# Optimization experiments

Hardware: AMD Instinct MI355X
Metric: run time of the kernel (lower is better)

Reference implementation:

```python
import jax, jax.numpy as jnp
import numpy as np

TAU = 2.0  # gumbel-softmax temperature (hard=False)


def setup_inputs() -> dict:
    key = jax.random.key(0)
    k = jax.random.split(key, 6)
    b = 128
    names = jax.random.normal(k[0], (b, 256, 30, 32), jnp.float32)
    patterns = jax.random.normal(k[1], (b, 4, 128, 128), jnp.float32)
    attributes = jax.random.normal(k[2], (b, 8, 15, 16), jnp.float32)
    palettes = jax.random.normal(k[3], (b, 8, 12), jnp.float32)
    u1 = jax.random.uniform(k[4], (b, 960, 256), jnp.float32, 1e-6, 1.0 - 1e-6)
    u2 = jax.random.uniform(k[5], (b, 240, 8), jnp.float32, 1e-6, 1.0 - 1e-6)
    gumbel_names = -jnp.log(-jnp.log(u1))
    gumbel_attrs = -jnp.log(-jnp.log(u2))
    return {"names": names, "patterns": patterns, "attributes": attributes,
            "palettes": palettes, "gumbel_names": gumbel_names, "gumbel_attrs": gumbel_attrs}


def reference(names, patterns, attributes, palettes, gumbel_names, gumbel_attrs):
    b = names.shape[0]
    # tile-name logits: (b,256,30,32) -> (b, 960 tiles, 256 names)
    n = names.reshape(b, 256, 30 * 32).transpose(0, 2, 1)
    names_idxs = jax.nn.softmax((n + gumbel_names) / TAU, axis=-1)
    # pattern table: (b,4,128,128) -> 256 tiles of 8x8 pixels x 4 gray levels
    p = patterns.reshape(b, 4, 16, 8, 16, 8).transpose(0, 2, 4, 3, 5, 1)
    p = jax.nn.softmax(p, axis=-1).reshape(b, 256, 8 * 8 * 4)
    # attribute logits: (b,8,15,16) -> (b, 240 blocks, 8 palettes)
    a = attributes.reshape(b, 8, 15 * 16).transpose(0, 2, 1)
    attributes_idxs = jax.nn.softmax((a + gumbel_attrs) / TAU, axis=-1)
    pal = palettes.reshape(b, 8, 4 * 3)
    # soft tile lookup: (b,960,256) @ (b,256,256) -> (b,960,256)
    monochrome = jnp.einsum('btn,bnp->btp', names_idxs, p)
    monochrome = monochrome.reshape(b, 30 * 32, 8 * 8, 4, 1)
    # soft palette lookup: (b,240,8) @ (b,8,12) -> (b,240,12)
    colorization = jnp.einsum('bte,bec->btc', attributes_idxs, pal)
    colorization = colorization.reshape(b, 15, 16, 4, 3)
    # 2x2 attribute-block broadcast to the 30x32 nametable
    colorization = jnp.repeat(jnp.repeat(colorization, 2, axis=1), 2, axis=2)
    colorization = colorization.reshape(b, 30 * 32, 1, 4, 3)
    colorized = (monochrome * colorization).sum(axis=3)  # (b,960,64,3)
    image = colorized.reshape(b, 30, 32, 8, 8, 3).transpose(0, 5, 1, 3, 2, 4)
    image = image.reshape(b, 3, 30 * 8, 32 * 8)
    image = jax.nn.sigmoid(image)
    return image, names_idxs, p, attributes_idxs, pal
```

## Files before the change

### kernel.cpp

```cpp
#include <hip/hip_runtime.h>
#include <hip/hip_bf16.h>
#include <math.h>

#define O_IMG   0
#define O_NAMES 23592960ULL
#define O_P     55050240ULL
#define O_ATTR  63438848ULL
#define O_PAL   63684608ULL

typedef __attribute__((ext_vector_type(8))) short short8v;
typedef __attribute__((ext_vector_type(4))) float f32x4;

static __device__ inline unsigned short f2bf(float x) {
    __hip_bfloat16 h = __float2bfloat16(x);
    return *reinterpret_cast<unsigned short*>(&h);
}

template<bool WRITE_PT>
__global__ __launch_bounds__(256) void k_pattern2(const float* __restrict__ patterns,
                                                  float* __restrict__ out_p,
                                                  unsigned short* __restrict__ Pt) {
    int bp = blockIdx.x;
    int b  = bp >> 3;
    int pi = bp & 7;

    __shared__ float sP[4 * 16 * 136];
    __shared__ unsigned short sR[32 * 264];

    int tid = threadIdx.x;

    #pragma unroll
    for (int p = 0; p < 8; p++) {
        int li   = p * 256 + tid;
        int col4 = li & 31;
        int ti   = (li >> 5) & 15;
        int g    = li >> 9;
        float4 v = *(const float4*)(patterns + (size_t)b * 65536 + g * 16384 +
                                    (ti * 8 + pi) * 128 + col4 * 4);
        *(float4*)&sP[(g * 16 + ti) * 136 + col4 * 4] = v;
    }
    __syncthreads();

    int pj = tid & 7;
    int nb = tid >> 3;
    #pragma unroll
    for (int i = 0; i < 8; i++) {
        int n  = nb * 8 + i;
        int ti = n >> 4, tj = n & 15;
        int base = ti * 136 + tj * 8 + pj;
        float v0 = sP[              base];
        float v1 = sP[16 * 136   + base];
        float v2 = sP[32 * 136   + base];
        float v3 = sP[48 * 136   + base];
        float m  = fmaxf(fmaxf(v0, v1), fmaxf(v2, v3));
        float e0 = __expf(v0 - m), e1 = __expf(v1 - m), e2 = __expf(v2 - m), e3 = __expf(v3 - m);
        float inv = 1.0f / (e0 + e1 + e2 + e3);
        float p0 = e0 * inv, p1 = e1 * inv, p2 = e2 * inv, p3 = e3 * inv;
        float4 r; r.x = p0; r.y = p1; r.z = p2; r.w = p3;
        *(float4*)(out_p + (size_t)(b * 256 + n) * 256 + pi * 32 + pj * 4) = r;
        if (WRITE_PT) {
            sR[(pj * 4 + 0) * 264 + n] = f2bf(p0);
            sR[(pj * 4 + 1) * 264 + n] = f2bf(p1);
            sR[(pj * 4 + 2) * 264 + n] = f2bf(p2);
            sR[(pj * 4 + 3) * 264 + n] = f2bf(p3);
        }
    }
    if (WRITE_PT) {
        __syncthreads();
        int n4  = tid & 63;
        int fl0 = tid >> 6;
        #pragma unroll
        for (int k = 0; k < 8; k++) {
            int fl = fl0 * 8 + k;
            short4 rv = *(short4*)&sR[fl * 264 + n4 * 4];
            *(short4*)(Pt + (size_t)b * 65536 + (size_t)(pi * 32 + fl) * 256 + n4 * 4) = rv;
        }
    }
}

__global__ __launch_bounds__(256) void k_names(const float* __restrict__ names,
                                               const float* __restrict__ gumbel,
                                               float* __restrict__ out) {
    int chunk = blockIdx.x % 60;
    int b     = blockIdx.x / 60;
    int t0 = chunk * 16;
    __shared__ float sN[256 * 17];

    int q = threadIdx.x;
    const float* nb = names + (size_t)b * 245760 + t0;
    {
        int j  = q & 3;
        int n0 = q >> 2;
        #pragma unroll
        for (int pass = 0; pass < 4; pass++) {
            int n = n0 + 64 * pass;
            float4 v = *(const float4*)(nb + (size_t)n * 960 + 4 * j);
            float* dst = sN + n * 17 + 4 * j;
            dst[0] = v.x; dst[1] = v.y; dst[2] = v.z; dst[3] = v.w;
        }
    }
    __syncthreads();

    int lane = q & 63;
    int w    = q >> 6;
    const float* gb = gumbel + ((size_t)b * 960 + t0) * 256;
    float*       ob = out    + ((size_t)b * 960 + t0) * 256;

    #pragma unroll
    for (int tt = 0; tt < 4; tt++) {
        int t = w * 4 + tt;
        float v[4];
        #pragma unroll
        for (int k = 0; k < 4; k++) {
            int n = lane + 64 * k;
            v[k] = (sN[n * 17 + t] + gb[(size_t)t * 256 + n]) * 0.5f;
        }
        float m = fmaxf(fmaxf(v[0], v[1]), fmaxf(v[2], v[3]));
        #pragma unroll
        for (int off = 1; off < 64; off <<= 1) m = fmaxf(m, __shfl_xor(m, off));
        float s = 0.f;
        #pragma unroll
        for (int k = 0; k < 4; k++) { v[k] = expf(v[k] - m); s += v[k]; }
        #pragma unroll
        for (int off = 1; off < 64; off <<= 1) s += __shfl_xor(s, off);
        float inv = 1.0f / s;
        #pragma unroll
        for (int k = 0; k < 4; k++) ob[(size_t)t * 256 + lane + 64 * k] = v[k] * inv;
    }
}

__global__ __launch_bounds__(256) void k_attr(const float* __restrict__ attributes,
                                              const float* __restrict__ gumbel,
                                              const float* __restrict__ palettes,
                                              float* __restrict__ out_attr,
                                              float* __restrict__ out_pal) {
    int idx = blockIdx.x * 256 + threadIdx.x;
    if (idx < 12288) out_pal[idx] = palettes[idx];
    if (idx >= 128 * 240) return;
    int tb = idx % 240;
    int b  = idx / 240;
    float v[8];
    float m = -1e30f;
    #pragma unroll
    for (int e = 0; e < 8; e++) {
        v[e] = (attributes[((size_t)b * 8 + e) * 240 + tb] +
                gumbel[((size_t)b * 240 + tb) * 8 + e]) * 0.5f;
        m = fmaxf(m, v[e]);
    }
    float s = 0.f;
    #pragma unroll
    for (int e = 0; e < 8; e++) { v[e] = __expf(v[e] - m); s += v[e]; }
    float inv = 1.0f / s;
    float* o = out_attr + (size_t)idx * 8;
    #pragma unroll
    for (int e = 0; e < 8; e++) o[e] = v[e] * inv;
}

__global__ __launch_bounds__(256, 4) void k_fused(const float* __restrict__ names,
                                                  const float* __restrict__ gumbel,
                                                  const unsigned short* __restrict__ Pt,
                                                  const float* __restrict__ attr,
                                                  const float* __restrict__ pal,
                                                  float* __restrict__ out_names,
                                                  float* __restrict__ img) {
    int j  = blockIdx.x;
    int x  = j & 7;
    int s  = j >> 3;
    int q  = s / 30;
    int rr = s % 30;
    int b  = x + 8 * q;
    int t0 = rr * 32;

    __shared__ __align__(16) char smem[16896];
    __shared__ float sN[256 * 17];
    __shared__ float sCol[192];

    int tid  = threadIdx.x;
    int lane = tid & 63;
    int w    = tid >> 6;
    int lo   = lane & 15;
    int hi   = lane >> 4;

    if (tid < 192) {
        int tbl = tid / 12;
        int gc  = tid % 12;
        int tb  = (rr >> 1) * 16 + tbl;
        const float* at = attr + ((size_t)b * 240 + tb) * 8;
        const float* pl = pal + (size_t)b * 96 + gc;
        float sum = 0.f;
        #pragma unroll
        for (int e = 0; e < 8; e++) sum += at[e] * pl[e * 12];
        sCol[tbl * 12 + gc] = sum;
    }

    const float* nb  = names + (size_t)b * 245760 + t0;
    const float* gb  = gumbel + ((size_t)b * 960 + t0) * 256;
    float*       onb = out_names + ((size_t)b * 960 + t0) * 256;

    for (int c = 0; c < 2; c++) {
        if (c) __syncthreads();
        {
            int jj = tid & 3;
            int n0 = tid >> 2;
            #pragma unroll
            for (int p = 0; p < 4; p++) {
                int n = n0 + 64 * p;
                float4 v = *(const float4*)(nb + (size_t)n * 960 + c * 16 + 4 * jj);
                float* dst = sN + n * 17 + 4 * jj;
                dst[0] = v.x; dst[1] = v.y; dst[2] = v.z; dst[3] = v.w;
            }
        }
        __syncthreads();
        #pragma unroll
        for (int tt = 0; tt < 4; tt++) {
            int trow = w * 4 + tt;
            int tl   = c * 16 + trow;
            float v[4];
            #pragma unroll
            for (int k = 0; k < 4; k++) {
                int n = lane + 64 * k;
                v[k] = (sN[n * 17 + trow] + gb[(size_t)tl * 256 + n]) * 0.5f;
            }
            float m = fmaxf(fmaxf(v[0], v[1]), fmaxf(v[2], v[3]));
            #pragma unroll
            for (int off = 1; off < 64; off <<= 1) m = fmaxf(m, __shfl_xor(m, off));
            float sm = 0.f;
            #pragma unroll
            for (int k = 0; k < 4; k++) { v[k] = __expf(v[k] - m); sm += v[k]; }
            #pragma unroll
            for (int off = 1; off < 64; off <<= 1) sm += __shfl_xor(sm, off);
            float inv = 1.0f / sm;
            #pragma unroll
            for (int k = 0; k < 4; k++) {
                int n = lane + 64 * k;
                float p = v[k] * inv;
                onb[(size_t)tl * 256 + n] = p;
                *(unsigned short*)(smem + ((tl * 512 + n * 2) ^ ((tl & 7) << 4))) = f2bf(p);
            }
        }
    }
    __syncthreads();

    f32x4 acc[2][4];
    #pragma unroll
    for (int mi = 0; mi < 2; mi++)
        #pragma unroll
        for (int ni = 0; ni < 4; ni++) acc[mi][ni] = (f32x4){0.f, 0.f, 0.f, 0.f};

    const unsigned short* Ptb = Pt + (size_t)b * 65536 + hi * 8;

    short8v bcur[4], bnxt[4];
    #pragma unroll
    for (int ni = 0; ni < 4; ni++) {
        int f = w * 64 + ni * 16 + lo;
        bcur[ni] = *(const short8v*)(Ptb + (size_t)f * 256);
    }

    #pragma unroll
    for (int k0 = 0; k0 < 256; k0 += 32) {
        if (k0 < 224) {
            #pragma unroll
            for (int ni = 0; ni < 4; ni++) {
                int f = w * 64 + ni * 16 + lo;
                bnxt[ni] = *(const short8v*)(Ptb + (size_t)f * 256 + k0 + 32);
            }
        }
        int ka = (k0 + hi * 8) * 2;
        short8v a0 = *(short8v*)(smem + (((lo      ) * 512 + ka) ^ ((lo & 7) << 4)));
        short8v a1 = *(short8v*)(smem + (((lo + 16) * 512 + ka) ^ ((lo & 7) << 4)));
        #pragma unroll
        for (int ni = 0; ni < 4; ni++) {
            acc[0][ni] = __builtin_amdgcn_mfma_f32_16x16x32_bf16(a0, bcur[ni], acc[0][ni], 0, 0, 0);
            acc[1][ni] = __builtin_amdgcn_mfma_f32_16x16x32_bf16(a1, bcur[ni], acc[1][ni], 0, 0, 0);
        }
        if (k0 < 224) {
            #pragma unroll
            for (int ni = 0; ni < 4; ni++) bcur[ni] = bnxt[ni];
        }
    }

    float* sMono = (float*)smem;
    int tf = tid & 63;
    int tm = tid >> 6;
    int pi = tf >> 3, pj = tf & 7;

    #pragma unroll
    for (int mi = 0; mi < 2; mi++) {
        __syncthreads();
        #pragma unroll
        for (int ni = 0; ni < 4; ni++) {
            int colf = w * 64 + ni * 16 + lo;
            #pragma unroll
            for (int rg = 0; rg < 4; rg++)
                sMono[(hi * 4 + rg) * 260 + colf] = acc[mi][ni][rg];
        }
        __syncthreads();
        int cbase = mi * 16;
        #pragma unroll
        for (int i = 0; i < 4; i++) {
            int ccl  = tm * 4 + i;
            int ccol = cbase + ccl;
            int tbl  = ccol >> 1;
            float4 mv = *(float4*)&sMono[ccl * 260 + tf * 4];
            #pragma unroll
            for (int c = 0; c < 3; c++) {
                float sv = mv.x * sCol[tbl * 12 + c]
                         + mv.y * sCol[tbl * 12 + 3 + c]
                         + mv.z * sCol[tbl * 12 + 6 + c]
                         + mv.w * sCol[tbl * 12 + 9 + c];
                float y = 1.0f / (1.0f + __expf(-sv));
                img[(((size_t)b * 3 + c) * 240 + rr * 8 + pi) * 256 + ccol * 8 + pj] = y;
            }
        }
    }
}

__global__ __launch_bounds__(256) void k_image_fp32(const float* __restrict__ A,
                                                    const float* __restrict__ P,
                                                    const float* __restrict__ attr,
                                                    const float* __restrict__ pal,
                                                    float* __restrict__ img) {
    int blk = blockIdx.x;
    int r = blk % 30;
    int b = blk / 30;
    int t0 = r * 32;

    __shared__ float sA[32][33];
    __shared__ float sB[32][256];
    __shared__ float sColF[16][12];

    int tid = threadIdx.x;
    if (tid < 192) {
        int tbl = tid / 12;
        int gc  = tid % 12;
        int tb  = (r >> 1) * 16 + tbl;
        const float* at = attr + ((size_t)b * 240 + tb) * 8;
        const float* pl = pal + (size_t)b * 96 + gc;
        float s = 0.f;
        #pragma unroll
        for (int e = 0; e < 8; e++) s += at[e] * pl[e * 12];
        sColF[tbl][gc] = s;
    }

    float acc[8][4];
    #pragma unroll
    for (int i = 0; i < 8; i++)
        #pragma unroll
        for (int j = 0; j < 4; j++) acc[i][j] = 0.f;

    int tf = tid & 63;
    int tm = tid >> 6;

    const float* Ab = A + ((size_t)b * 960 + t0) * 256;
    const float* Pb = P + (size_t)b * 65536;

    for (int k0 = 0; k0 < 256; k0 += 32) {
        __syncthreads();
        #pragma unroll
        for (int i = 0; i < 4; i++) {
            int li = tid + i * 256;
            int tl = li >> 5, kk = li & 31;
            sA[tl][kk] = Ab[(size_t)tl * 256 + k0 + kk];
        }
        #pragma unroll
        for (int i = 0; i < 8; i++) {
            int li = tid + i * 256;
            int kk = li >> 6, ff = (li & 63) * 4;
            *(float4*)&sB[kk][ff] = *(const float4*)&Pb[(size_t)(k0 + kk) * 256 + ff];
        }
        __syncthreads();
        #pragma unroll
        for (int kk = 0; kk < 32; kk++) {
            float4 bv = *(float4*)&sB[kk][tf * 4];
            #pragma unroll
            for (int i = 0; i < 8; i++) {
                float av = sA[tm * 8 + i][kk];
                acc[i][0] += av * bv.x;
                acc[i][1] += av * bv.y;
                acc[i][2] += av * bv.z;
                acc[i][3] += av * bv.w;
            }
        }
    }

    int pi = tf >> 3, pj = tf & 7;
    #pragma unroll
    for (int i = 0; i < 8; i++) {
        int cc  = tm * 8 + i;
        int tbl = cc >> 1;
        #pragma unroll
        for (int c = 0; c < 3; c++) {
            float s = acc[i][0] * sColF[tbl][c]
                    + acc[i][1] * sColF[tbl][3 + c]
                    + acc[i][2] * sColF[tbl][6 + c]
                    + acc[i][3] * sColF[tbl][9 + c];
            float y = 1.0f / (1.0f + expf(-s));
            img[(((size_t)b * 3 + c) * 240 + r * 8 + pi) * 256 + cc * 8 + pj] = y;
        }
    }
}

extern "C" void kernel_launch(void* const* d_in, const int* in_sizes, int n_in,
                              void* d_out, int out_size, void* d_ws, size_t ws_size,
                              hipStream_t stream) {
    const float* names       = (const float*)d_in[0];
    const float* patterns    = (const float*)d_in[1];
    const float* attributes  = (const float*)d_in[2];
    const float* palettes    = (const float*)d_in[3];
    const float* gumbel_n    = (const float*)d_in[4];
    const float* gumbel_a    = (const float*)d_in[5];
    float* out = (float*)d_out;

    float* out_img   = out + O_IMG;
    float* out_names = out + O_NAMES;
    float* out_p     = out + O_P;
    float* out_attr  = out + O_ATTR;
    float* out_pal   = out + O_PAL;

    const size_t PT_BYTES = 128ULL * 256 * 256 * 2;
    bool use_mfma = (ws_size >= PT_BYTES) && (d_ws != nullptr);

    if (use_mfma) {
        unsigned short* Pt = (unsigned short*)d_ws;
        k_pattern2<true><<<1024, 256, 0, stream>>>(patterns, out_p, Pt);
        k_attr<<<120, 256, 0, stream>>>(attributes, gumbel_a, palettes, out_attr, out_pal);
        k_fused<<<3840, 256, 0, stream>>>(names, gumbel_n, Pt, out_attr, palettes,
                                          out_names, out_img);
    } else {
        k_pattern2<false><<<1024, 256, 0, stream>>>(patterns, out_p, nullptr);
        k_names<<<128 * 60, 256, 0, stream>>>(names, gumbel_n, out_names);
        k_attr<<<120, 256, 0, stream>>>(attributes, gumbel_a, palettes, out_attr, out_pal);
        k_image_fp32<<<128 * 30, 256, 0, stream>>>(out_names, out_p, out_attr, palettes, out_img);
    }
}
```

Before: 169.9 us.

## Split names softmax from MFMA image kernel via bf16 workspace staging

Un-fuses the names softmax from the image GEMM. A separate k_names2 kernel writes both the fp32 output and a swizzled bf16 copy to workspace. k_image2 then bulk-loads that bf16 tile into shared memory and computes 64 tiles per block, two nametable rows with 4x4 MFMA accumulators, over half as many blocks. This aims to raise occupancy and reuse of each B fragment in the GEMM. In exchange it adds an extra kernel launch, a global round trip of about 63 MB of bf16 probabilities, and a larger workspace requirement with a fallback path.

```diff
diff --git a/kernel.cpp b/kernel.cpp
--- a/kernel.cpp
+++ b/kernel.cpp
@@ -78,9 +78,10 @@
     }
 }
 
-__global__ __launch_bounds__(256) void k_names(const float* __restrict__ names,
-                                               const float* __restrict__ gumbel,
-                                               float* __restrict__ out) {
+__global__ __launch_bounds__(256) void k_names2(const float* __restrict__ names,
+                                                const float* __restrict__ gumbel,
+                                                float* __restrict__ out,
+                                                char* __restrict__ wsA) {
     int chunk = blockIdx.x % 60;
     int b     = blockIdx.x / 60;
     int t0 = chunk * 16;
@@ -105,6 +106,7 @@
     int w    = q >> 6;
     const float* gb = gumbel + ((size_t)b * 960 + t0) * 256;
     float*       ob = out    + ((size_t)b * 960 + t0) * 256;
+    char*        wa = wsA + (size_t)b * 491520;
 
     #pragma unroll
     for (int tt = 0; tt < 4; tt++) {
@@ -120,12 +122,18 @@
         for (int off = 1; off < 64; off <<= 1) m = fmaxf(m, __shfl_xor(m, off));
         float s = 0.f;
         #pragma unroll
-        for (int k = 0; k < 4; k++) { v[k] = expf(v[k] - m); s += v[k]; }
+        for (int k = 0; k < 4; k++) { v[k] = __expf(v[k] - m); s += v[k]; }
         #pragma unroll
         for (int off = 1; off < 64; off <<= 1) s += __shfl_xor(s, off);
         float inv = 1.0f / s;
-        #pragma unroll
-        for (int k = 0; k < 4; k++) ob[(size_t)t * 256 + lane + 64 * k] = v[k] * inv;
+        int tg = t0 + t;
+        #pragma unroll
+        for (int k = 0; k < 4; k++) {
+            int n = lane + 64 * k;
+            float p = v[k] * inv;
+            ob[(size_t)t * 256 + n] = p;
+            *(unsigned short*)(wa + (((size_t)tg * 512 + n * 2) ^ ((tg & 7) << 4))) = f2bf(p);
+        }
     }
 }
 
@@ -156,23 +164,20 @@
     for (int e = 0; e < 8; e++) o[e] = v[e] * inv;
 }
 
-__global__ __launch_bounds__(256, 4) void k_fused(const float* __restrict__ names,
-                                                  const float* __restrict__ gumbel,
-                                                  const unsigned short* __restrict__ Pt,
-                                                  const float* __restrict__ attr,
-                                                  const float* __restrict__ pal,
-                                                  float* __restrict__ out_names,
-                                                  float* __restrict__ img) {
+__global__ __launch_bounds__(256, 4) void k_image2(const char* __restrict__ wsA,
+                                                   const unsigned short* __restrict__ Pt,
+                                                   const float* __restrict__ attr,
+                                                   const float* __restrict__ pal,
+                                                   float* __restrict__ img) {
     int j  = blockIdx.x;
     int x  = j & 7;
     int s  = j >> 3;
-    int q  = s / 30;
-    int rr = s % 30;
+    int q  = s / 15;
+    int rr = s % 15;
     int b  = x + 8 * q;
-    int t0 = rr * 32;
-
-    __shared__ __align__(16) char smem[16896];
-    __shared__ float sN[256 * 17];
+    int t0 = rr * 64;
+
+    __shared__ __align__(16) char smem[32768];
     __shared__ float sCol[192];
 
     int tid  = threadIdx.x;
@@ -184,7 +189,7 @@
     if (tid < 192) {
         int tbl = tid / 12;
         int gc  = tid % 12;
-        int tb  = (rr >> 1) * 16 + tbl;
+        int tb  = rr * 16 + tbl;
         const float* at = attr + ((size_t)b * 240 + tb) * 8;
         const float* pl = pal + (size_t)b * 96 + gc;
         float sum = 0.f;
@@ -193,57 +198,19 @@
         sCol[tbl * 12 + gc] = sum;
     }
 
-    const float* nb  = names + (size_t)b * 245760 + t0;
-    const float* gb  = gumbel + ((size_t)b * 960 + t0) * 256;
-    float*       onb = out_names + ((size_t)b * 960 + t0) * 256;
-
-    for (int c = 0; c < 2; c++) {
-        if (c) __syncthreads();
-        {
-            int jj = tid & 3;
-            int n0 = tid >> 2;
-            #pragma unroll
-            for (int p = 0; p < 4; p++) {
-                int n = n0 + 64 * p;
-                float4 v = *(const float4*)(nb + (size_t)n * 960 + c * 16 + 4 * jj);
-                float* dst = sN + n * 17 + 4 * jj;
-                dst[0] = v.x; dst[1] = v.y; dst[2] = v.z; dst[3] = v.w;
-            }
-        }
-        __syncthreads();
-        #pragma unroll
-        for (int tt = 0; tt < 4; tt++) {
-            int trow = w * 4 + tt;
-            int tl   = c * 16 + trow;
-            float v[4];
-            #pragma unroll
-            for (int k = 0; k < 4; k++) {
-                int n = lane + 64 * k;
-                v[k] = (sN[n * 17 + trow] + gb[(size_t)tl * 256 + n]) * 0.5f;
-            }
-            float m = fmaxf(fmaxf(v[0], v[1]), fmaxf(v[2], v[3]));
-            #pragma unroll
-            for (int off = 1; off < 64; off <<= 1) m = fmaxf(m, __shfl_xor(m, off));
-            float sm = 0.f;
-            #pragma unroll
-            for (int k = 0; k < 4; k++) { v[k] = __expf(v[k] - m); sm += v[k]; }
-            #pragma unroll
-            for (int off = 1; off < 64; off <<= 1) sm += __shfl_xor(sm, off);
-            float inv = 1.0f / sm;
-            #pragma unroll
-            for (int k = 0; k < 4; k++) {
-                int n = lane + 64 * k;
-                float p = v[k] * inv;
-                onb[(size_t)tl * 256 + n] = p;
-                *(unsigned short*)(smem + ((tl * 512 + n * 2) ^ ((tl & 7) << 4))) = f2bf(p);
-            }
+    {
+        const char* src = wsA + (size_t)b * 491520 + (size_t)t0 * 512;
+        #pragma unroll
+        for (int i = 0; i < 8; i++) {
+            int off = (i * 256 + tid) * 16;
+            *(short8v*)(smem + off) = *(const short8v*)(src + off);
         }
     }
     __syncthreads();
 
-    f32x4 acc[2][4];
-    #pragma unroll
-    for (int mi = 0; mi < 2; mi++)
+    f32x4 acc[4][4];
+    #pragma unroll
+    for (int mi = 0; mi < 4; mi++)
         #pragma unroll
         for (int ni = 0; ni < 4; ni++) acc[mi][ni] = (f32x4){0.f, 0.f, 0.f, 0.f};
 
@@ -268,10 +235,14 @@
         int ka = (k0 + hi * 8) * 2;
         short8v a0 = *(short8v*)(smem + (((lo      ) * 512 + ka) ^ ((lo & 7) << 4)));
         short8v a1 = *(short8v*)(smem + (((lo + 16) * 512 + ka) ^ ((lo & 7) << 4)));
+        short8v a2 = *(short8v*)(smem + (((lo + 32) * 512 + ka) ^ ((lo & 7) << 4)));
+        short8v a3 = *(short8v*)(smem + (((lo + 48) * 512 + ka) ^ ((lo & 7) << 4)));
         #pragma unroll
         for (int ni = 0; ni < 4; ni++) {
             acc[0][ni] = __builtin_amdgcn_mfma_f32_16x16x32_bf16(a0, bcur[ni], acc[0][ni], 0, 0, 0);
             acc[1][ni] = __builtin_amdgcn_mfma_f32_16x16x32_bf16(a1, bcur[ni], acc[1][ni], 0, 0, 0);
+            acc[2][ni] = __builtin_amdgcn_mfma_f32_16x16x32_bf16(a2, bcur[ni], acc[2][ni], 0, 0, 0);
+            acc[3][ni] = __builtin_amdgcn_mfma_f32_16x16x32_bf16(a3, bcur[ni], acc[3][ni], 0, 0, 0);
         }
         if (k0 < 224) {
             #pragma unroll
@@ -285,7 +256,7 @@
     int pi = tf >> 3, pj = tf & 7;
 
     #pragma unroll
-    for (int mi = 0; mi < 2; mi++) {
+    for (int mi = 0; mi < 4; mi++) {
         __syncthreads();
         #pragma unroll
         for (int ni = 0; ni < 4; ni++) {
@@ -295,7 +266,8 @@
                 sMono[(hi * 4 + rg) * 260 + colf] = acc[mi][ni][rg];
         }
         __syncthreads();
-        int cbase = mi * 16;
+        int r     = rr * 2 + (mi >> 1);
+        int cbase = (mi & 1) * 16;
         #pragma unroll
         for (int i = 0; i < 4; i++) {
             int ccl  = tm * 4 + i;
@@ -309,9 +281,60 @@
                          + mv.z * sCol[tbl * 12 + 6 + c]
                          + mv.w * sCol[tbl * 12 + 9 + c];
                 float y = 1.0f / (1.0f + __expf(-sv));
-                img[(((size_t)b * 3 + c) * 240 + rr * 8 + pi) * 256 + ccol * 8 + pj] = y;
+                img[(((size_t)b * 3 + c) * 240 + r * 8 + pi) * 256 + ccol * 8 + pj] = y;
             }
         }
+    }
+}
+
+__global__ __launch_bounds__(256) void k_names(const float* __restrict__ names,
+                                               const float* __restrict__ gumbel,
+                                               float* __restrict__ out) {
+    int chunk = blockIdx.x % 60;
+    int b     = blockIdx.x / 60;
+    int t0 = chunk * 16;
+    __shared__ float sN[256 * 17];
+
+    int q = threadIdx.x;
+    const float* nb = names + (size_t)b * 245760 + t0;
+    {
+        int j  = q & 3;
+        int n0 = q >> 2;
+        #pragma unroll
+        for (int pass = 0; pass < 4; pass++) {
+            int n = n0 + 64 * pass;
+            float4 v = *(const float4*)(nb + (size_t)n * 960 + 4 * j);
+            float* dst = sN + n * 17 + 4 * j;
+            dst[0] = v.x; dst[1] = v.y; dst[2] = v.z; dst[3] = v.w;
+        }
+    }
+    __syncthreads();
+
+    int lane = q & 63;
+    int w    = q >> 6;
+    const float* gb = gumbel + ((size_t)b * 960 + t0) * 256;
+    float*       ob = out    + ((size_t)b * 960 + t0) * 256;
+
+    #pragma unroll
+    for (int tt = 0; tt < 4; tt++) {
+        int t = w * 4 + tt;
+        float v[4];
+        #pragma unroll
+        for (int k = 0; k < 4; k++) {
+            int n = lane + 64 * k;
+            v[k] = (sN[n * 17 + t] + gb[(size_t)t * 256 + n]) * 0.5f;
+        }
+        float m = fmaxf(fmaxf(v[0], v[1]), fmaxf(v[2], v[3]));
+        #pragma unroll
+        for (int off = 1; off < 64; off <<= 1) m = fmaxf(m, __shfl_xor(m, off));
+        float s = 0.f;
+        #pragma unroll
+        for (int k = 0; k < 4; k++) { v[k] = expf(v[k] - m); s += v[k]; }
+        #pragma unroll
+        for (int off = 1; off < 64; off <<= 1) s += __shfl_xor(s, off);
+        float inv = 1.0f / s;
+        #pragma unroll
+        for (int k = 0; k < 4; k++) ob[(size_t)t * 256 + lane + 64 * k] = v[k] * inv;
     }
 }
 
@@ -418,14 +441,23 @@
     float* out_pal   = out + O_PAL;
 
     const size_t PT_BYTES = 128ULL * 256 * 256 * 2;
-    bool use_mfma = (ws_size >= PT_BYTES) && (d_ws != nullptr);
-
-    if (use_mfma) {
+    const size_t A_BYTES  = 128ULL * 960 * 256 * 2;
+    bool use_split = (ws_size >= PT_BYTES + A_BYTES) && (d_ws != nullptr);
+    bool use_pt    = (ws_size >= PT_BYTES) && (d_ws != nullptr);
+
+    if (use_split) {
+        unsigned short* Pt = (unsigned short*)d_ws;
+        char* wsA = (char*)d_ws + PT_BYTES;
+        k_pattern2<true><<<1024, 256, 0, stream>>>(patterns, out_p, Pt);
+        k_attr<<<120, 256, 0, stream>>>(attributes, gumbel_a, palettes, out_attr, out_pal);
+        k_names2<<<128 * 60, 256, 0, stream>>>(names, gumbel_n, out_names, wsA);
+        k_image2<<<1920, 256, 0, stream>>>(wsA, Pt, out_attr, palettes, out_img);
+    } else if (use_pt) {
         unsigned short* Pt = (unsigned short*)d_ws;
         k_pattern2<true><<<1024, 256, 0, stream>>>(patterns, out_p, Pt);
+        k_names<<<128 * 60, 256, 0, stream>>>(names, gumbel_n, out_names);
         k_attr<<<120, 256, 0, stream>>>(attributes, gumbel_a, palettes, out_attr, out_pal);
-        k_fused<<<3840, 256, 0, stream>>>(names, gumbel_n, Pt, out_attr, palettes,
-                                          out_names, out_img);
+        k_image_fp32<<<128 * 30, 256, 0, stream>>>(out_names, out_p, out_attr, palettes, out_img);
     } else {
         k_pattern2<false><<<1024, 256, 0, stream>>>(patterns, out_p, nullptr);
         k_names<<<128 * 60, 256, 0, stream>>>(names, gumbel_n, out_names);
```

After: 198.0 us. 16.6% more time.
